# Optimization experiments

Hardware: AMD Instinct MI355X
Metric: run time of the kernel (lower is better)

## Reference

```python
import jax, jax.numpy as jnp
import numpy as np

THR = 0.6
EPS = 1e-12


def _mlp(x, w1, b1, w2, b2):
    # Linear -> ReLU -> (Dropout eval = identity) -> Linear
    return jax.nn.relu(x @ w1 + b1) @ w2 + b2


def setup_inputs() -> dict:
    B, H, D = 16384, 1024, 300
    key = jax.random.key(0)
    ks = jax.random.split(key, 32)
    s = 0.02
    inp = {
        'brics': jax.random.normal(ks[0], (B, H), jnp.float32),
        'function_group': jax.random.normal(ks[1], (B, H), jnp.float32),
        'pharmacophore': jax.random.normal(ks[2], (B, H), jnp.float32),
        # fingerprint encoders (brics / function_group / pharmacophore)
        'bw1': jax.random.normal(ks[3], (H, D), jnp.float32) * s,
        'bb1': jnp.zeros((D,), jnp.float32),
        'bw2': jax.random.normal(ks[4], (D, H), jnp.float32) * s,
        'bb2': jnp.zeros((H,), jnp.float32),
        'fw1': jax.random.normal(ks[5], (H, D), jnp.float32) * s,
        'fb1': jnp.zeros((D,), jnp.float32),
        'fw2': jax.random.normal(ks[6], (D, H), jnp.float32) * s,
        'fb2': jnp.zeros((H,), jnp.float32),
        'pw1': jax.random.normal(ks[7], (H, D), jnp.float32) * s,
        'pb1': jnp.zeros((D,), jnp.float32),
        'pw2': jax.random.normal(ks[8], (D, H), jnp.float32) * s,
        'pb2': jnp.zeros((H,), jnp.float32),
        # weight generator: Linear(3H, 3)
        'wg_W': jax.random.normal(ks[9], (3 * H, 3), jnp.float32) * s,
        'wg_b': jnp.zeros((3,), jnp.float32),
        # enhancement layer: Linear(H, H) + sigmoid
        'enh_W': jax.random.normal(ks[10], (H, H), jnp.float32) * s,
        'enh_b': jnp.zeros((H,), jnp.float32),
        # fusion layer: Linear(2H, H)
        'fus_W': jax.random.normal(ks[11], (2 * H, H), jnp.float32) * s,
        'fus_b': jnp.zeros((H,), jnp.float32),
    }
    return inp


def reference(brics, function_group, pharmacophore,
              bw1, bb1, bw2, bb2,
              fw1, fb1, fw2, fb2,
              pw1, pb1, pw2, pb2,
              wg_W, wg_b, enh_W, enh_b, fus_W, fus_b):
    B, H = brics.shape
    eb = _mlp(brics, bw1, bb1, bw2, bb2)            # [B,H]
    ef = _mlp(function_group, fw1, fb1, fw2, fb2)   # [B,H]
    ep = _mlp(pharmacophore, pw1, pb1, pw2, pb2)    # [B,H]

    E = jnp.stack([eb, ef, ep], axis=1)             # [B,3,H]
    En = E / jnp.maximum(jnp.linalg.norm(E, axis=-1, keepdims=True), EPS)

    # three unordered pairs (0,1),(0,2),(1,2); softmax-weighted sum is
    # permutation invariant, so the original python sort is a no-op.
    ii = jnp.array([0, 0, 1])
    jj = jnp.array([1, 2, 2])
    Ei, Ej = E[:, ii], E[:, jj]                     # [B,3,H]
    Eni, Enj = En[:, ii], En[:, jj]
    sim = jnp.sum(Eni * Enj, axis=-1)               # [B,3] cosine sims
    keep = sim > THR                                # pairs above threshold

    elem_mask = (Eni * Enj > THR).astype(E.dtype)   # [B,3,H]
    cf = 0.5 * (Ei + Ej) * elem_mask                # candidate common feats

    w = jax.nn.softmax(jnp.where(keep, sim, -1e9), axis=-1)  # [B,3]
    wsum = jnp.einsum('bp,bph->bh', w, cf)
    mean_fp = jnp.mean(E, axis=1)
    any_kept = jnp.any(keep, axis=-1, keepdims=True)
    common = jnp.where(any_kept, wsum, mean_fp)     # [B,H]

    all_cat = jnp.concatenate([eb, ef, ep], axis=1)          # [B,3H]
    fp_w = jax.nn.softmax(all_cat @ wg_W + wg_b, axis=1)     # [B,3]
    weighted_fp_sum = jnp.einsum('bk,bkh->bh', fp_w, E)

    enh = jax.nn.sigmoid(common @ enh_W + enh_b)
    enhanced_common = common * enh

    fused = jnp.concatenate([weighted_fp_sum, enhanced_common], axis=1) @ fus_W + fus_b
    return fused
```

## Files before the change

kernel.cpp:

```cpp
#include <hip/hip_runtime.h>
#include <stdint.h>


typedef __attribute__((ext_vector_type(8))) __bf16 bf16x8;
typedef __attribute__((ext_vector_type(8))) short short8;
typedef __attribute__((ext_vector_type(4))) float floatx4;

__device__ __forceinline__ uint16_t f2bf(float f) {
  __bf16 h = (__bf16)f;
  return __builtin_bit_cast(uint16_t, h);
}
__device__ __forceinline__ float bf2f(uint16_t h) {
  union { uint32_t u; float f; } v; v.u = ((uint32_t)h) << 16;
  return v.f;
}
__device__ __forceinline__ short8 pack8(float4 a, float4 b) {
  union { __bf16 h[8]; short8 s; } u;
  u.h[0] = (__bf16)a.x; u.h[1] = (__bf16)a.y; u.h[2] = (__bf16)a.z; u.h[3] = (__bf16)a.w;
  u.h[4] = (__bf16)b.x; u.h[5] = (__bf16)b.y; u.h[6] = (__bf16)b.z; u.h[7] = (__bf16)b.w;
  return u.s;
}
__device__ __forceinline__ void gload16(const void* g, void* l) {
  __builtin_amdgcn_global_load_lds(
      (const __attribute__((address_space(1))) void*)g,
      (__attribute__((address_space(3))) void*)l, 16, 0, 0);
}

__global__ void cfe_transpose_all(const float* __restrict__ bw1, const float* __restrict__ fw1,
                                  const float* __restrict__ pw1, const float* __restrict__ bw2,
                                  const float* __restrict__ fw2, const float* __restrict__ pw2,
                                  const float* __restrict__ enhW, const float* __restrict__ fusW,
                                  uint16_t* __restrict__ W1T, uint16_t* __restrict__ W2T,
                                  uint16_t* __restrict__ ENHT, uint16_t* __restrict__ FUST) {
  int bid = blockIdx.x;
  const float* src; uint16_t* dst; int K, N, Kpad, Npad, bx, by;
  if (bid < 1152) {
    int z = bid / 384, t = bid % 384; bx = t % 32; by = t / 32;
    src = (z == 0) ? bw1 : ((z == 1) ? fw1 : pw1); dst = W1T + (long)z * 384 * 1024;
    K = 1024; N = 300; Kpad = 1024; Npad = 384;
  } else if (bid < 2112) {
    bid -= 1152; int z = bid / 320, t = bid % 320; bx = t % 10; by = t / 10;
    src = (z == 0) ? bw2 : ((z == 1) ? fw2 : pw2); dst = W2T + (long)z * 1024 * 320;
    K = 300; N = 1024; Kpad = 320; Npad = 1024;
  } else if (bid < 3136) {
    bid -= 2112; bx = bid % 32; by = bid / 32;
    src = enhW; dst = ENHT; K = 1024; N = 1024; Kpad = 1024; Npad = 1024;
  } else {
    bid -= 3136; bx = bid % 64; by = bid / 64;
    src = fusW; dst = FUST; K = 2048; N = 1024; Kpad = 2048; Npad = 1024;
  }
  __shared__ float tile[32][33];
  const int tx = threadIdx.x & 31;
  const int ty = threadIdx.x >> 5;
  const int k0 = bx * 32;
  const int n0 = by * 32;
#pragma unroll
  for (int i = 0; i < 4; i++) {
    int k = k0 + ty + 8 * i;
    int n = n0 + tx;
    tile[ty + 8 * i][tx] = (k < K && n < N) ? src[(long)k * N + n] : 0.f;
  }
  __syncthreads();
#pragma unroll
  for (int i = 0; i < 4; i++) {
    int n = n0 + ty + 8 * i;
    int k = k0 + tx;
    if (n < Npad && k < Kpad) dst[(long)n * Kpad + k] = f2bf(tile[tx][ty + 8 * i]);
  }
}

template <int MODE, int AF32>
__global__ void cfe_gemm128(const void* __restrict__ A0, const void* __restrict__ A1,
                            const void* __restrict__ A2, int lda,
                            const uint16_t* __restrict__ Bt, long sBz, int ldb,
                            void* __restrict__ C, long sCz, int ldc, int colofs,
                            const float* __restrict__ bias0,
                            const float* __restrict__ bias1,
                            const float* __restrict__ bias2, int biasN,
                            const uint16_t* __restrict__ common, int K) {
  const int z = blockIdx.z;
  const void* Av = (z == 0) ? A0 : ((z == 1) ? A1 : A2);
  Bt += (long)z * sBz;
  const float* bias = (z == 0) ? bias0 : ((z == 1) ? bias1 : bias2);

  const int gx = gridDim.x;
  const int lin = blockIdx.y * gx + blockIdx.x;
  const int P = (gx * gridDim.y) >> 3;
  const int v = (lin & 7) * P + (lin >> 3);
  const long bm = (long)(v / gx) * 128;
  const long bn = (long)(v % gx) * 128;

  const int tid = threadIdx.x;
  const int wave = tid >> 6;
  const int lane = tid & 63;
  const int wm = wave >> 1;
  const int wn = wave & 1;

  __shared__ __attribute__((aligned(16))) uint16_t As[AF32 ? 128 * 64 : 128 * 32];
  __shared__ __attribute__((aligned(16))) uint16_t Bs[128 * 32];

  floatx4 acc[4][4];
#pragma unroll
  for (int i = 0; i < 4; i++)
#pragma unroll
    for (int j = 0; j < 4; j++) acc[i][j] = (floatx4){0.f, 0.f, 0.f, 0.f};

  const int lrow = lane >> 2;
  const int lcolB = (((lane & 3) ^ ((lrow >> 1) & 3)) * 8);
  const uint16_t* Bp = Bt + (bn + wave * 32 + lrow) * (long)ldb + lcolB;
  uint16_t* BsW0 = &Bs[(wave * 32) * 32];
  uint16_t* BsW1 = &Bs[(wave * 32 + 16) * 32];
  const uint16_t* Ap = nullptr;
  uint16_t* AsW0 = &As[(wave * 32) * 32];
  uint16_t* AsW1 = &As[(wave * 32 + 16) * 32];
  if constexpr (!AF32) {
    Ap = (const uint16_t*)Av + (bm + wave * 32 + lrow) * (long)lda + lcolB;
  }

  const float* ApS = nullptr;
  char* AsB = nullptr;
  if constexpr (AF32) {
    const int r_in = lane >> 3;
    const int gpos = (lane & 7) >> 1;
    const int halfp = lane & 1;
    const int scol = ((gpos ^ (r_in & 3)) << 3) | ((halfp ^ ((r_in >> 2) & 1)) << 2);
    ApS = (const float*)Av + (bm + wave * 32 + r_in) * (long)lda + scol;
    AsB = (char*)As + (wave * 32) * 128;
  }

  const int fr = lane & 15;
  const int fq = lane >> 4;
  const int swr = (fr >> 1) & 3;
  const uint16_t* ArBase = &As[(wm * 64 + fr) * 32 + (fq ^ swr) * 8];
  const uint16_t* BrBase = &Bs[(wn * 64 + fr) * 32 + (fq ^ swr) * 8];
  const int ga = fq ^ (fr & 3);
  const int hb = (fr >> 2) & 1;
  const float* AfBase = (const float*)As + (wm * 64 + fr) * 32 + ga * 8;

  for (int k0 = 0; k0 < K; k0 += 32) {
    if constexpr (AF32) {
      gload16(ApS + k0, AsB);
      gload16(ApS + 8 * (long)lda + k0, AsB + 1024);
      gload16(ApS + 16 * (long)lda + k0, AsB + 2048);
      gload16(ApS + 24 * (long)lda + k0, AsB + 3072);
    } else {
      gload16(Ap + k0, AsW0);
      gload16(Ap + 16 * (long)lda + k0, AsW1);
    }
    gload16(Bp + k0, BsW0);
    gload16(Bp + 16 * (long)ldb + k0, BsW1);
    __syncthreads();

    short8 a[4], b[4];
    if constexpr (AF32) {
#pragma unroll
      for (int mi = 0; mi < 4; mi++) {
        const float* Af = AfBase + mi * 512;
        float4 lo = *(const float4*)(Af + hb * 4);
        float4 hi = *(const float4*)(Af + (hb ^ 1) * 4);
        a[mi] = pack8(lo, hi);
      }
    } else {
#pragma unroll
      for (int mi = 0; mi < 4; mi++) a[mi] = *(const short8*)(ArBase + mi * 512);
    }
#pragma unroll
    for (int ni = 0; ni < 4; ni++) b[ni] = *(const short8*)(BrBase + ni * 512);
#pragma unroll
    for (int mi = 0; mi < 4; mi++)
#pragma unroll
      for (int ni = 0; ni < 4; ni++)
        acc[mi][ni] = __builtin_amdgcn_mfma_f32_16x16x32_bf16(
            __builtin_bit_cast(bf16x8, a[mi]), __builtin_bit_cast(bf16x8, b[ni]),
            acc[mi][ni], 0, 0, 0);
    __syncthreads();
  }

#pragma unroll
  for (int mi = 0; mi < 4; mi++) {
    long row = bm + wm * 64 + mi * 16 + fq * 4;
#pragma unroll
    for (int ni = 0; ni < 4; ni++) {
      long col = bn + wn * 64 + ni * 16 + fr;
      float bv = (col < biasN) ? bias[col] : 0.f;
#pragma unroll
      for (int r = 0; r < 4; r++) {
        float vv = acc[mi][ni][r] + bv;
        long idx = (row + r) * (long)ldc + colofs + col;
        if constexpr (MODE == 0) {
          ((uint16_t*)C)[(long)z * sCz + idx] = f2bf(fmaxf(vv, 0.f));
        } else if constexpr (MODE == 1) {
          ((uint16_t*)C)[(long)z * sCz + idx] = f2bf(vv);
        } else if constexpr (MODE == 2) {
          float c = bf2f(common[(row + r) * 1024 + col]);
          float s = 1.f / (1.f + __expf(-vv));
          ((uint16_t*)C)[idx] = f2bf(c * s);
        } else {
          ((float*)C)[idx] = vv;
        }
      }
    }
  }
}

__global__ void cfe_pointwise_kernel(const uint16_t* __restrict__ E,
                                     const float* __restrict__ wgW,
                                     const float* __restrict__ wgb,
                                     uint16_t* __restrict__ commonb,
                                     uint16_t* __restrict__ fusedA) {
  const int row = blockIdx.x;
  const int tid = threadIdx.x;
  const long ES = 16384L * 1024;
  const long base = (long)row * 1024 + tid * 4;

  ushort4 u0 = *(const ushort4*)(E + base);
  ushort4 u1 = *(const ushort4*)(E + ES + base);
  ushort4 u2 = *(const ushort4*)(E + 2 * ES + base);
  float eb[4] = {bf2f(u0.x), bf2f(u0.y), bf2f(u0.z), bf2f(u0.w)};
  float ef[4] = {bf2f(u1.x), bf2f(u1.y), bf2f(u1.z), bf2f(u1.w)};
  float ep[4] = {bf2f(u2.x), bf2f(u2.y), bf2f(u2.z), bf2f(u2.w)};

  float vals[9];
#pragma unroll
  for (int i = 0; i < 9; i++) vals[i] = 0.f;
#pragma unroll
  for (int j = 0; j < 4; j++) {
    int h = tid * 4 + j;
    vals[0] += eb[j] * eb[j];
    vals[1] += ef[j] * ef[j];
    vals[2] += ep[j] * ep[j];
    vals[3] += eb[j] * ef[j];
    vals[4] += eb[j] * ep[j];
    vals[5] += ef[j] * ep[j];
#pragma unroll
    for (int c = 0; c < 3; c++)
      vals[6 + c] += eb[j] * wgW[(long)h * 3 + c] +
                     ef[j] * wgW[(long)(1024 + h) * 3 + c] +
                     ep[j] * wgW[(long)(2048 + h) * 3 + c];
  }

#pragma unroll
  for (int i = 0; i < 9; i++) {
    float v = vals[i];
    for (int off = 32; off; off >>= 1) v += __shfl_down(v, off);
    vals[i] = v;
  }
  __shared__ float red[4][9];
  if ((tid & 63) == 0) {
#pragma unroll
    for (int i = 0; i < 9; i++) red[tid >> 6][i] = vals[i];
  }
  __syncthreads();
  float tot[9];
#pragma unroll
  for (int i = 0; i < 9; i++)
    tot[i] = red[0][i] + red[1][i] + red[2][i] + red[3][i];

  const float EPSF = 1e-12f;
  float nb = fmaxf(sqrtf(tot[0]), EPSF);
  float nf = fmaxf(sqrtf(tot[1]), EPSF);
  float np_ = fmaxf(sqrtf(tot[2]), EPSF);
  float s01 = tot[3] / (nb * nf);
  float s02 = tot[4] / (nb * np_);
  float s12 = tot[5] / (nf * np_);
  bool k01 = s01 > 0.6f, k02 = s02 > 0.6f, k12 = s12 > 0.6f;
  bool any = k01 | k02 | k12;
  float z0 = k01 ? s01 : -1e9f;
  float z1 = k02 ? s02 : -1e9f;
  float z2 = k12 ? s12 : -1e9f;
  float zm = fmaxf(z0, fmaxf(z1, z2));
  float w0 = __expf(z0 - zm), w1 = __expf(z1 - zm), w2 = __expf(z2 - zm);
  float wsum = w0 + w1 + w2;
  w0 /= wsum; w1 /= wsum; w2 /= wsum;

  float g0 = tot[6] + wgb[0], g1 = tot[7] + wgb[1], g2 = tot[8] + wgb[2];
  float gm = fmaxf(g0, fmaxf(g1, g2));
  float f0 = __expf(g0 - gm), f1 = __expf(g1 - gm), f2 = __expf(g2 - gm);
  float fs = f0 + f1 + f2;
  f0 /= fs; f1 /= fs; f2 /= fs;

  float inb = 1.f / nb, inf_ = 1.f / nf, inp = 1.f / np_;
  ushort4 co, wf;
  uint16_t cov[4], wfv[4];
#pragma unroll
  for (int j = 0; j < 4; j++) {
    float b = eb[j], f = ef[j], p = ep[j];
    float nbv = b * inb, nfv = f * inf_, npv = p * inp;
    float c01 = (nbv * nfv > 0.6f) ? 0.5f * (b + f) : 0.f;
    float c02 = (nbv * npv > 0.6f) ? 0.5f * (b + p) : 0.f;
    float c12 = (nfv * npv > 0.6f) ? 0.5f * (f + p) : 0.f;
    float ws = w0 * c01 + w1 * c02 + w2 * c12;
    float cm = any ? ws : (b + f + p) * (1.f / 3.f);
    float wfs = f0 * b + f1 * f + f2 * p;
    cov[j] = f2bf(cm);
    wfv[j] = f2bf(wfs);
  }
  co.x = cov[0]; co.y = cov[1]; co.z = cov[2]; co.w = cov[3];
  wf.x = wfv[0]; wf.y = wfv[1]; wf.z = wfv[2]; wf.w = wfv[3];
  *(ushort4*)(commonb + base) = co;
  *(ushort4*)(fusedA + (long)row * 2048 + tid * 4) = wf;
}

extern "C" void kernel_launch(void* const* d_in, const int* in_sizes, int n_in,
                              void* d_out, int out_size, void* d_ws, size_t ws_size,
                              hipStream_t stream) {
  (void)in_sizes; (void)n_in; (void)out_size; (void)ws_size;
  const float* brics = (const float*)d_in[0];
  const float* fg    = (const float*)d_in[1];
  const float* ph    = (const float*)d_in[2];
  const float* bw1 = (const float*)d_in[3];  const float* bb1 = (const float*)d_in[4];
  const float* bw2 = (const float*)d_in[5];  const float* bb2 = (const float*)d_in[6];
  const float* fw1 = (const float*)d_in[7];  const float* fb1 = (const float*)d_in[8];
  const float* fw2 = (const float*)d_in[9];  const float* fb2 = (const float*)d_in[10];
  const float* pw1 = (const float*)d_in[11]; const float* pb1 = (const float*)d_in[12];
  const float* pw2 = (const float*)d_in[13]; const float* pb2 = (const float*)d_in[14];
  const float* wgW = (const float*)d_in[15]; const float* wgb = (const float*)d_in[16];
  const float* enhW = (const float*)d_in[17]; const float* enhb = (const float*)d_in[18];
  const float* fusW = (const float*)d_in[19]; const float* fusb = (const float*)d_in[20];
  float* out = (float*)d_out;

  uint16_t* EB   = (uint16_t*)d_ws;
  uint16_t* FA   = EB + 3L * 16384 * 1024;
  uint16_t* W1T  = FA + 16384L * 2048;
  uint16_t* W2T  = W1T + 3L * 384 * 1024;
  uint16_t* ENHT = W2T + 3L * 1024 * 320;
  uint16_t* FUST = ENHT + 1024L * 1024;
  uint16_t* YB   = (uint16_t*)d_out;
  uint16_t* COM  = (uint16_t*)d_out;

  cfe_transpose_all<<<5184, 256, 0, stream>>>(
      bw1, fw1, pw1, bw2, fw2, pw2, enhW, fusW, W1T, W2T, ENHT, FUST);

  cfe_gemm128<0, 1><<<dim3(3, 128, 3), 256, 0, stream>>>(
      brics, fg, ph, 1024, W1T, 384L * 1024, 1024,
      YB, 16384L * 384, 384, 0, bb1, fb1, pb1, 300, nullptr, 1024);

  cfe_gemm128<1, 0><<<dim3(8, 128, 3), 256, 0, stream>>>(
      YB, YB + 16384L * 384, YB + 2 * 16384L * 384, 384, W2T, 1024L * 320, 320,
      EB, 16384L * 1024, 1024, 0, bb2, fb2, pb2, 1024, nullptr, 320);

  cfe_pointwise_kernel<<<16384, 256, 0, stream>>>(EB, wgW, wgb, COM, FA);

  cfe_gemm128<2, 0><<<dim3(8, 128, 1), 256, 0, stream>>>(
      COM, COM, COM, 1024, ENHT, 0, 1024,
      FA, 0, 2048, 1024, enhb, enhb, enhb, 1024, COM, 1024);

  cfe_gemm128<3, 0><<<dim3(8, 128, 1), 256, 0, stream>>>(
      FA, FA, FA, 2048, FUST, 0, 2048,
      out, 0, 1024, 0, fusb, fusb, fusb, 1024, nullptr, 2048);
}
```

Measured before the change: 562.0 us.

## Double-buffer LDS tiles to overlap global loads with MFMA compute

The GEMM kernel's shared-memory A and B tiles are doubled so the next K-slice is loaded directly into LDS while the current slice feeds the MFMAs. Explicit vmcnt waits and raw s_barrier calls replace the two __syncthreads per iteration. The goal is to hide global-to-LDS latency behind compute. In exchange, LDS usage doubles, which may lower occupancy, and the hand-counted vmcnt values must match the number of outstanding loads exactly.

Measured after the change: 545.9 us. 1.03x faster.

```diff
diff --git a/kernel.cpp b/kernel.cpp
--- a/kernel.cpp
+++ b/kernel.cpp
@@ -96,8 +96,10 @@
   const int wm = wave >> 1;
   const int wn = wave & 1;
 
-  __shared__ __attribute__((aligned(16))) uint16_t As[AF32 ? 128 * 64 : 128 * 32];
-  __shared__ __attribute__((aligned(16))) uint16_t Bs[128 * 32];
+  constexpr int ASZ16 = AF32 ? 128 * 64 : 128 * 32;
+  constexpr int BSZ16 = 128 * 32;
+  __shared__ __attribute__((aligned(16))) uint16_t As[2 * ASZ16];
+  __shared__ __attribute__((aligned(16))) uint16_t Bs[2 * BSZ16];
 
   floatx4 acc[4][4];
 #pragma unroll
@@ -108,25 +110,36 @@
   const int lrow = lane >> 2;
   const int lcolB = (((lane & 3) ^ ((lrow >> 1) & 3)) * 8);
   const uint16_t* Bp = Bt + (bn + wave * 32 + lrow) * (long)ldb + lcolB;
-  uint16_t* BsW0 = &Bs[(wave * 32) * 32];
-  uint16_t* BsW1 = &Bs[(wave * 32 + 16) * 32];
   const uint16_t* Ap = nullptr;
-  uint16_t* AsW0 = &As[(wave * 32) * 32];
-  uint16_t* AsW1 = &As[(wave * 32 + 16) * 32];
   if constexpr (!AF32) {
     Ap = (const uint16_t*)Av + (bm + wave * 32 + lrow) * (long)lda + lcolB;
   }
 
   const float* ApS = nullptr;
-  char* AsB = nullptr;
   if constexpr (AF32) {
     const int r_in = lane >> 3;
     const int gpos = (lane & 7) >> 1;
     const int halfp = lane & 1;
     const int scol = ((gpos ^ (r_in & 3)) << 3) | ((halfp ^ ((r_in >> 2) & 1)) << 2);
     ApS = (const float*)Av + (bm + wave * 32 + r_in) * (long)lda + scol;
-    AsB = (char*)As + (wave * 32) * 128;
-  }
+  }
+
+  auto stage = [&](int k0, int p) {
+    if constexpr (AF32) {
+      char* AsBp = (char*)As + p * (ASZ16 * 2) + (wave * 32) * 128;
+      gload16(ApS + k0, AsBp);
+      gload16(ApS + 8 * (long)lda + k0, AsBp + 1024);
+      gload16(ApS + 16 * (long)lda + k0, AsBp + 2048);
+      gload16(ApS + 24 * (long)lda + k0, AsBp + 3072);
+    } else {
+      uint16_t* AsP = As + p * ASZ16 + (wave * 32) * 32;
+      gload16(Ap + k0, AsP);
+      gload16(Ap + 16 * (long)lda + k0, AsP + 16 * 32);
+    }
+    uint16_t* BsP = Bs + p * BSZ16 + (wave * 32) * 32;
+    gload16(Bp + k0, BsP);
+    gload16(Bp + 16 * (long)ldb + k0, BsP + 16 * 32);
+  };
 
   const int fr = lane & 15;
   const int fq = lane >> 4;
@@ -137,35 +150,25 @@
   const int hb = (fr >> 2) & 1;
   const float* AfBase = (const float*)As + (wm * 64 + fr) * 32 + ga * 8;
 
-  for (int k0 = 0; k0 < K; k0 += 32) {
-    if constexpr (AF32) {
-      gload16(ApS + k0, AsB);
-      gload16(ApS + 8 * (long)lda + k0, AsB + 1024);
-      gload16(ApS + 16 * (long)lda + k0, AsB + 2048);
-      gload16(ApS + 24 * (long)lda + k0, AsB + 3072);
-    } else {
-      gload16(Ap + k0, AsW0);
-      gload16(Ap + 16 * (long)lda + k0, AsW1);
-    }
-    gload16(Bp + k0, BsW0);
-    gload16(Bp + 16 * (long)ldb + k0, BsW1);
-    __syncthreads();
-
+  auto compute_tile = [&](int p) {
     short8 a[4], b[4];
     if constexpr (AF32) {
+      const float* Af = AfBase + p * (ASZ16 / 2);
 #pragma unroll
       for (int mi = 0; mi < 4; mi++) {
-        const float* Af = AfBase + mi * 512;
-        float4 lo = *(const float4*)(Af + hb * 4);
-        float4 hi = *(const float4*)(Af + (hb ^ 1) * 4);
+        const float* Afm = Af + mi * 512;
+        float4 lo = *(const float4*)(Afm + hb * 4);
+        float4 hi = *(const float4*)(Afm + (hb ^ 1) * 4);
         a[mi] = pack8(lo, hi);
       }
     } else {
-#pragma unroll
-      for (int mi = 0; mi < 4; mi++) a[mi] = *(const short8*)(ArBase + mi * 512);
+      const uint16_t* Ar = ArBase + p * ASZ16;
+#pragma unroll
+      for (int mi = 0; mi < 4; mi++) a[mi] = *(const short8*)(Ar + mi * 512);
     }
-#pragma unroll
-    for (int ni = 0; ni < 4; ni++) b[ni] = *(const short8*)(BrBase + ni * 512);
+    const uint16_t* Br = BrBase + p * BSZ16;
+#pragma unroll
+    for (int ni = 0; ni < 4; ni++) b[ni] = *(const short8*)(Br + ni * 512);
 #pragma unroll
     for (int mi = 0; mi < 4; mi++)
 #pragma unroll
@@ -173,8 +176,28 @@
         acc[mi][ni] = __builtin_amdgcn_mfma_f32_16x16x32_bf16(
             __builtin_bit_cast(bf16x8, a[mi]), __builtin_bit_cast(bf16x8, b[ni]),
             acc[mi][ni], 0, 0, 0);
-    __syncthreads();
-  }
+  };
+
+  const int nt = K >> 5;
+  int pb = 0;
+  stage(0, 0);
+  for (int t = 0; t + 1 < nt; ++t, pb ^= 1) {
+    stage((t + 1) << 5, pb ^ 1);
+    if constexpr (AF32) {
+      asm volatile("s_waitcnt vmcnt(6)" ::: "memory");
+    } else {
+      asm volatile("s_waitcnt vmcnt(4)" ::: "memory");
+    }
+    __builtin_amdgcn_s_barrier();
+    __builtin_amdgcn_sched_barrier(0);
+    compute_tile(pb);
+    __builtin_amdgcn_sched_barrier(0);
+    __builtin_amdgcn_s_barrier();
+  }
+  asm volatile("s_waitcnt vmcnt(0)" ::: "memory");
+  __builtin_amdgcn_s_barrier();
+  __builtin_amdgcn_sched_barrier(0);
+  compute_tile(pb);
 
 #pragma unroll
   for (int mi = 0; mi < 4; mi++) {
```
